# Optimization experiments

Measured on AMD Instinct MI355X. Metric: run time of the kernel, lower is better.

Reference implementation:

```python
import jax, jax.numpy as jnp
import numpy as np

N_NODES = 50000
D = 64            # encoder.out_node_dim
N_EDGES = 800000
HID = 64          # mlp_edge_model_dim


def setup_inputs() -> dict:
    key = jax.random.key(0)
    k1, k2, k3, k4 = jax.random.split(key, 4)
    node_emb = jax.random.normal(k1, (N_NODES, D), dtype=jnp.float32)
    edge_index = jax.random.randint(k2, (2, N_EDGES), 0, N_NODES, dtype=jnp.int64)
    # Xavier-uniform style init for the 2-layer edge MLP
    lim1 = np.sqrt(6.0 / (2 * D + HID)).astype(np.float32)
    lim2 = np.sqrt(6.0 / (HID + 1)).astype(np.float32)
    W1 = jax.random.uniform(k3, (2 * D, HID), minval=-lim1, maxval=lim1, dtype=jnp.float32)
    b1 = jnp.zeros((HID,), dtype=jnp.float32)
    W2 = jax.random.uniform(k4, (HID, 1), minval=-lim2, maxval=lim2, dtype=jnp.float32)
    b2 = jnp.zeros((1,), dtype=jnp.float32)
    return {"node_emb": node_emb, "edge_index": edge_index,
            "W1": W1, "b1": b1, "W2": W2, "b2": b2}


def reference(node_emb, edge_index, W1, b1, W2, b2):
    src, dst = edge_index[0], edge_index[1]
    emb_src = node_emb[src]              # [E, D] gather
    emb_dst = node_emb[dst]              # [E, D] gather
    edge_emb = jnp.concatenate([emb_src, emb_dst], axis=1)  # [E, 2D]
    h = jax.nn.relu(edge_emb @ W1 + b1)  # [E, HID]
    edge_logits = h @ W2 + b2            # [E, 1]
    return edge_logits
```

## Files before the change

kernel.cpp:

```cpp
#include <hip/hip_runtime.h>


typedef __attribute__((ext_vector_type(8))) short short8;
typedef __attribute__((ext_vector_type(4))) float f32x4;

__device__ __forceinline__ unsigned short f2bf_rne(float f) {
    union { float f; unsigned u; } v;
    v.f = f;
    return (unsigned short)((v.u + 0x7FFFu + ((v.u >> 16) & 1u)) >> 16);
}

__global__ void cvt_to_bf16(const float* __restrict__ x,
                            unsigned short* __restrict__ y, int n4) {
    int i = blockIdx.x * blockDim.x + threadIdx.x;
    if (i >= n4) return;
    f32x4 v = ((const f32x4*)x)[i];
    ushort4 o;
    o.x = f2bf_rne(v[0]);
    o.y = f2bf_rne(v[1]);
    o.z = f2bf_rne(v[2]);
    o.w = f2bf_rne(v[3]);
    ((ushort4*)y)[i] = o;
}

#define W1T_STRIDE 136

struct Rows { short8 a0, a1, a2, a3; };

__device__ __forceinline__ Rows load_rows(const unsigned short* __restrict__ nodebf,
                                          int src, int dst, int ko) {
    Rows r;
    const unsigned short* rs = nodebf + (size_t)src * 64;
    const unsigned short* rd = nodebf + (size_t)dst * 64;
    r.a0 = *(const short8*)(rs + ko);
    r.a1 = *(const short8*)(rs + 32 + ko);
    r.a2 = *(const short8*)(rd + ko);
    r.a3 = *(const short8*)(rd + 32 + ko);
    return r;
}

__global__ __launch_bounds__(256, 3)
void edge_mlp(const int* __restrict__ eidx,
              const unsigned short* __restrict__ nodebf,
              const float* __restrict__ W1,
              const float* __restrict__ b1,
              const float* __restrict__ W2,
              const float* __restrict__ b2,
              float* __restrict__ out,
              int E, int ntiles) {
    __shared__ __align__(16) unsigned short w1t[64 * W1T_STRIDE];

    const int tid = threadIdx.x;

#pragma unroll
    for (int i = 0; i < 32; ++i) {
        int idx = tid + i * 256;
        int k = idx >> 6;
        int n = idx & 63;
        w1t[n * W1T_STRIDE + k] = f2bf_rne(W1[idx]);
    }
    __syncthreads();

    const int lane = tid & 63;
    const int wid = tid >> 6;
    const int c = lane & 15;
    const int quad = lane >> 4;
    const int ko = quad * 8;

    short8 bfrag[4][4];
#pragma unroll
    for (int nt = 0; nt < 4; ++nt)
#pragma unroll
        for (int kc = 0; kc < 4; ++kc)
            bfrag[nt][kc] =
                *(const short8*)&w1t[(nt * 16 + c) * W1T_STRIDE + kc * 32 + quad * 8];

    float w2v[4], b1v[4];
#pragma unroll
    for (int nt = 0; nt < 4; ++nt) {
        w2v[nt] = W2[nt * 16 + c];
        b1v[nt] = b1[nt * 16 + c];
    }
    const float b2v = b2[0];

    const int stride = gridDim.x * 4;
    int t = blockIdx.x * 4 + wid;
    int tn = t + stride;

    int snxt = 0, dnxt = 0;
    Rows cur;
    if (t < ntiles) {
        int e = t * 16 + c;
        int ec = (e < E) ? e : (E - 1);
        int s = eidx[ec], d = eidx[E + ec];
        cur = load_rows(nodebf, s, d, ko);
        if (tn < ntiles) {
            int en = tn * 16 + c;
            int enc = (en < E) ? en : (E - 1);
            snxt = eidx[enc];
            dnxt = eidx[E + enc];
        }
    }

    for (; t < ntiles; t += stride, tn += stride) {
        const bool has_next = (tn < ntiles);
        Rows nxt;
        if (has_next) nxt = load_rows(nodebf, snxt, dnxt, ko);

        int t2 = tn + stride;
        int s2 = 0, d2 = 0;
        if (t2 < ntiles) {
            int e2 = t2 * 16 + c;
            int e2c = (e2 < E) ? e2 : (E - 1);
            s2 = eidx[e2c];
            d2 = eidx[E + e2c];
        }

        f32x4 acc[4];
#pragma unroll
        for (int nt = 0; nt < 4; ++nt) acc[nt] = (f32x4){0.f, 0.f, 0.f, 0.f};
#pragma unroll
        for (int nt = 0; nt < 4; ++nt) {
            acc[nt] = __builtin_amdgcn_mfma_f32_16x16x32_bf16(cur.a0, bfrag[nt][0], acc[nt], 0, 0, 0);
            acc[nt] = __builtin_amdgcn_mfma_f32_16x16x32_bf16(cur.a1, bfrag[nt][1], acc[nt], 0, 0, 0);
            acc[nt] = __builtin_amdgcn_mfma_f32_16x16x32_bf16(cur.a2, bfrag[nt][2], acc[nt], 0, 0, 0);
            acc[nt] = __builtin_amdgcn_mfma_f32_16x16x32_bf16(cur.a3, bfrag[nt][3], acc[nt], 0, 0, 0);
        }

        float p[4];
#pragma unroll
        for (int r = 0; r < 4; ++r) p[r] = 0.f;
#pragma unroll
        for (int nt = 0; nt < 4; ++nt)
#pragma unroll
            for (int r = 0; r < 4; ++r) {
                float h = fmaxf(acc[nt][r] + b1v[nt], 0.f);
                p[r] = fmaf(h, w2v[nt], p[r]);
            }
#pragma unroll
        for (int m = 1; m < 16; m <<= 1)
#pragma unroll
            for (int r = 0; r < 4; ++r) p[r] += __shfl_xor(p[r], m, 16);

        if (c == 0) {
            int base = t * 16 + quad * 4;
            if (base + 3 < E) {
                f32x4 o = {p[0] + b2v, p[1] + b2v, p[2] + b2v, p[3] + b2v};
                *(f32x4*)(out + base) = o;
            } else {
#pragma unroll
                for (int r = 0; r < 4; ++r)
                    if (base + r < E) out[base + r] = p[r] + b2v;
            }
        }

        if (has_next) cur = nxt;
        snxt = s2;
        dnxt = d2;
    }
}

extern "C" void kernel_launch(void* const* d_in, const int* in_sizes, int n_in,
                              void* d_out, int out_size, void* d_ws, size_t ws_size,
                              hipStream_t stream) {
    const float* node = (const float*)d_in[0];
    const int* eidx = (const int*)d_in[1];
    const float* W1 = (const float*)d_in[2];
    const float* b1 = (const float*)d_in[3];
    const float* W2 = (const float*)d_in[4];
    const float* b2 = (const float*)d_in[5];
    float* out = (float*)d_out;

    const int node_elems = in_sizes[0];
    const int E = in_sizes[1] / 2;
    const int n4 = node_elems / 4;

    unsigned short* nodebf = (unsigned short*)d_ws;

    cvt_to_bf16<<<(n4 + 255) / 256, 256, 0, stream>>>(node, nodebf, n4);

    const int ntiles = (E + 15) / 16;
    edge_mlp<<<2048, 256, 0, stream>>>(eidx, nodebf, W1, b1, W2, b2, out, E, ntiles);
}
```

Before: 113.8 us.

## Process tile pairs per wave with ping-pong row buffers and halve grid

Each wave now owns two adjacent tiles per iteration and alternates between two register row buffers. The gather for one tile and the index fetch for the next are issued before the MFMA work on the other tile. This is meant to hide more gather latency behind compute. The grid is halved so the total tile coverage stays the same, at the cost of more live registers per thread and fewer resident waves.

```diff
diff --git a/kernel.cpp b/kernel.cpp
--- a/kernel.cpp
+++ b/kernel.cpp
@@ -37,6 +37,63 @@
     r.a2 = *(const short8*)(rd + ko);
     r.a3 = *(const short8*)(rd + 32 + ko);
     return r;
+}
+
+__device__ __forceinline__ int2 fetch_idx(const int* __restrict__ eidx, int E,
+                                          int t, int c) {
+    int e = t * 16 + c;
+    e = (e < E) ? e : (E - 1);
+    int2 r;
+    r.x = eidx[e];
+    r.y = eidx[E + e];
+    return r;
+}
+
+__device__ __forceinline__ void compute_tile(const Rows& rows,
+                                             const short8 (&bfrag)[4][4],
+                                             const float (&b1v)[4], const float (&w2v)[4],
+                                             float b2v, int t, int ntiles, int E,
+                                             int c, int quad,
+                                             float* __restrict__ out) {
+    if (t >= ntiles) return;
+
+    f32x4 acc[4];
+#pragma unroll
+    for (int nt = 0; nt < 4; ++nt) acc[nt] = (f32x4){0.f, 0.f, 0.f, 0.f};
+#pragma unroll
+    for (int nt = 0; nt < 4; ++nt) {
+        acc[nt] = __builtin_amdgcn_mfma_f32_16x16x32_bf16(rows.a0, bfrag[nt][0], acc[nt], 0, 0, 0);
+        acc[nt] = __builtin_amdgcn_mfma_f32_16x16x32_bf16(rows.a1, bfrag[nt][1], acc[nt], 0, 0, 0);
+        acc[nt] = __builtin_amdgcn_mfma_f32_16x16x32_bf16(rows.a2, bfrag[nt][2], acc[nt], 0, 0, 0);
+        acc[nt] = __builtin_amdgcn_mfma_f32_16x16x32_bf16(rows.a3, bfrag[nt][3], acc[nt], 0, 0, 0);
+    }
+
+    float p[4];
+#pragma unroll
+    for (int r = 0; r < 4; ++r) p[r] = 0.f;
+#pragma unroll
+    for (int nt = 0; nt < 4; ++nt)
+#pragma unroll
+        for (int r = 0; r < 4; ++r) {
+            float h = fmaxf(acc[nt][r] + b1v[nt], 0.f);
+            p[r] = fmaf(h, w2v[nt], p[r]);
+        }
+#pragma unroll
+    for (int m = 1; m < 16; m <<= 1)
+#pragma unroll
+        for (int r = 0; r < 4; ++r) p[r] += __shfl_xor(p[r], m, 16);
+
+    if (c == 0) {
+        int base = t * 16 + quad * 4;
+        if (base + 3 < E) {
+            f32x4 o = {p[0] + b2v, p[1] + b2v, p[2] + b2v, p[3] + b2v};
+            *(f32x4*)(out + base) = o;
+        } else {
+#pragma unroll
+            for (int r = 0; r < 4; ++r)
+                if (base + r < E) out[base + r] = p[r] + b2v;
+        }
+    }
 }
 
 __global__ __launch_bounds__(256, 3)
@@ -83,80 +140,22 @@
     }
     const float b2v = b2[0];
 
-    const int stride = gridDim.x * 4;
-    int t = blockIdx.x * 4 + wid;
-    int tn = t + stride;
+    const int S = gridDim.x * 4 * 2;
+    int t = (blockIdx.x * 4 + wid) * 2;
 
-    int snxt = 0, dnxt = 0;
-    Rows cur;
-    if (t < ntiles) {
-        int e = t * 16 + c;
-        int ec = (e < E) ? e : (E - 1);
-        int s = eidx[ec], d = eidx[E + ec];
-        cur = load_rows(nodebf, s, d, ko);
-        if (tn < ntiles) {
-            int en = tn * 16 + c;
-            int enc = (en < E) ? en : (E - 1);
-            snxt = eidx[enc];
-            dnxt = eidx[E + enc];
-        }
-    }
+    int2 iA = fetch_idx(eidx, E, t, c);
+    Rows rowsA = load_rows(nodebf, iA.x, iA.y, ko);
+    int2 iB = fetch_idx(eidx, E, t + 1, c);
+    Rows rowsB;
 
-    for (; t < ntiles; t += stride, tn += stride) {
-        const bool has_next = (tn < ntiles);
-        Rows nxt;
-        if (has_next) nxt = load_rows(nodebf, snxt, dnxt, ko);
+    for (; t < ntiles; t += S) {
+        rowsB = load_rows(nodebf, iB.x, iB.y, ko);
+        iA = fetch_idx(eidx, E, t + S, c);
+        compute_tile(rowsA, bfrag, b1v, w2v, b2v, t, ntiles, E, c, quad, out);
 
-        int t2 = tn + stride;
-        int s2 = 0, d2 = 0;
-        if (t2 < ntiles) {
-            int e2 = t2 * 16 + c;
-            int e2c = (e2 < E) ? e2 : (E - 1);
-            s2 = eidx[e2c];
-            d2 = eidx[E + e2c];
-        }
-
-        f32x4 acc[4];
-#pragma unroll
-        for (int nt = 0; nt < 4; ++nt) acc[nt] = (f32x4){0.f, 0.f, 0.f, 0.f};
-#pragma unroll
-        for (int nt = 0; nt < 4; ++nt) {
-            acc[nt] = __builtin_amdgcn_mfma_f32_16x16x32_bf16(cur.a0, bfrag[nt][0], acc[nt], 0, 0, 0);
-            acc[nt] = __builtin_amdgcn_mfma_f32_16x16x32_bf16(cur.a1, bfrag[nt][1], acc[nt], 0, 0, 0);
-            acc[nt] = __builtin_amdgcn_mfma_f32_16x16x32_bf16(cur.a2, bfrag[nt][2], acc[nt], 0, 0, 0);
-            acc[nt] = __builtin_amdgcn_mfma_f32_16x16x32_bf16(cur.a3, bfrag[nt][3], acc[nt], 0, 0, 0);
-        }
-
-        float p[4];
-#pragma unroll
-        for (int r = 0; r < 4; ++r) p[r] = 0.f;
-#pragma unroll
-        for (int nt = 0; nt < 4; ++nt)
-#pragma unroll
-            for (int r = 0; r < 4; ++r) {
-                float h = fmaxf(acc[nt][r] + b1v[nt], 0.f);
-                p[r] = fmaf(h, w2v[nt], p[r]);
-            }
-#pragma unroll
-        for (int m = 1; m < 16; m <<= 1)
-#pragma unroll
-            for (int r = 0; r < 4; ++r) p[r] += __shfl_xor(p[r], m, 16);
-
-        if (c == 0) {
-            int base = t * 16 + quad * 4;
-            if (base + 3 < E) {
-                f32x4 o = {p[0] + b2v, p[1] + b2v, p[2] + b2v, p[3] + b2v};
-                *(f32x4*)(out + base) = o;
-            } else {
-#pragma unroll
-                for (int r = 0; r < 4; ++r)
-                    if (base + r < E) out[base + r] = p[r] + b2v;
-            }
-        }
-
-        if (has_next) cur = nxt;
-        snxt = s2;
-        dnxt = d2;
+        rowsA = load_rows(nodebf, iA.x, iA.y, ko);
+        iB = fetch_idx(eidx, E, t + S + 1, c);
+        compute_tile(rowsB, bfrag, b1v, w2v, b2v, t + 1, ntiles, E, c, quad, out);
     }
 }
 
@@ -180,5 +179,5 @@
     cvt_to_bf16<<<(n4 + 255) / 256, 256, 0, stream>>>(node, nodebf, n4);
 
     const int ntiles = (E + 15) / 16;
-    edge_mlp<<<2048, 256, 0, stream>>>(eidx, nodebf, W1, b1, W2, b2, out, E, ntiles);
+    edge_mlp<<<1024, 256, 0, stream>>>(eidx, nodebf, W1, b1, W2, b2, out, E, ntiles);
 }
```

New measurement: 112.1 us. About the same (-1.5%).
